# Performance work log

Hardware: AMD Instinct MI355X
Metric: run time of the kernel (lower is better)

The kernel has to match this reference:

```python
import jax, jax.numpy as jnp
import numpy as np

NUM_CLASSES = 80
NUM_ANCHORS = 3  # len(anchor_mask)
STRIDE = 8.0
# anchors[mask=0,1,2] = (12,16),(19,36),(40,28), divided by stride
ANCHOR_W = jnp.array([12.0, 19.0, 40.0], dtype=jnp.float32) / STRIDE
ANCHOR_H = jnp.array([16.0, 36.0, 28.0], dtype=jnp.float32) / STRIDE


def setup_inputs() -> dict:
    key = jax.random.key(0)
    output = jax.random.normal(key, (16, NUM_ANCHORS * (5 + NUM_CLASSES), 76, 76), dtype=jnp.float32)
    return {"output": output}


def reference(output):
    B, C_total, H, W = output.shape
    A, C = NUM_ANCHORS, NUM_CLASSES
    o = output.reshape(B, A, 5 + C, H, W)

    bxy = jax.nn.sigmoid(o[:, :, 0:2])          # [B,A,2,H,W]
    bwh = jnp.exp(o[:, :, 2:4])                 # [B,A,2,H,W]
    det_confs = jax.nn.sigmoid(o[:, :, 4])      # [B,A,H,W]
    cls_confs = jax.nn.softmax(o[:, :, 5:], axis=2)  # softmax over class dim, [B,A,C,H,W]

    grid_x = jnp.arange(W, dtype=jnp.float32)[None, None, None, :]
    grid_y = jnp.arange(H, dtype=jnp.float32)[None, None, :, None]
    aw = ANCHOR_W[None, :, None, None]
    ah = ANCHOR_H[None, :, None, None]

    bx = (bxy[:, :, 0] + grid_x) / W            # [B,A,H,W]
    by = (bxy[:, :, 1] + grid_y) / H
    bw = (bwh[:, :, 0] * aw) / W
    bh = (bwh[:, :, 1] * ah) / H

    boxes = jnp.stack([bx, by, bw, bh], axis=-1).reshape(B, A * H * W, 4)
    cls_flat = cls_confs.transpose(0, 1, 3, 4, 2).reshape(B, A * H * W, C)
    confs = cls_flat * det_confs.reshape(B, A * H * W, 1)
    return boxes, confs
```

## Files before the change

### kernel.cpp

```cpp
#include <hip/hip_runtime.h>

#define HW_   5776
#define W_    76
#define NC_   80
#define NA_   3
#define NB_   16
#define NCH_  85

__device__ __forceinline__ float sigmoidf_(float x) {
    return 1.0f / (1.0f + __expf(-x));
}

__global__ __launch_bounds__(256) void yolo_kernel(const float* __restrict__ in,
                                                   float* __restrict__ out) {
    const int p = blockIdx.x * 256 + threadIdx.x;
    if (p >= HW_) return;
    const int a = blockIdx.y;
    const int b = blockIdx.z;

    const float aw3[3] = {1.5f, 2.375f, 5.0f};
    const float ah3[3] = {2.0f, 4.5f, 3.5f};
    const float invW = 1.0f / 76.0f;

    const float* src = in + (size_t)(b * NA_ + a) * NCH_ * HW_ + p;
    float v[NCH_];
#pragma unroll
    for (int ch = 0; ch < NCH_; ++ch) {
        v[ch] = src[(size_t)ch * HW_];
    }

    const int x = p % W_;
    const int y = p / W_;

    const float bx  = (sigmoidf_(v[0]) + (float)x) * invW;
    const float by  = (sigmoidf_(v[1]) + (float)y) * invW;
    const float bw  = __expf(v[2]) * (aw3[a] * invW);
    const float bh  = __expf(v[3]) * (ah3[a] * invW);
    const float det = sigmoidf_(v[4]);

    float m = v[5];
#pragma unroll
    for (int c = 1; c < NC_; ++c) m = fmaxf(m, v[5 + c]);
    float s = 0.0f;
#pragma unroll
    for (int c = 0; c < NC_; ++c) {
        v[5 + c] = __expf(v[5 + c] - m);
        s += v[5 + c];
    }
    const float scale = det / s;

    const size_t idx = (size_t)a * HW_ + (size_t)p;
    float4* boxout = (float4*)out + (size_t)b * (NA_ * HW_) + idx;
    *boxout = make_float4(bx, by, bw, bh);

    float* conf = out + (size_t)NB_ * NA_ * HW_ * 4
                      + ((size_t)b * (NA_ * HW_) + idx) * NC_;
#pragma unroll
    for (int c = 0; c < NC_; c += 4) {
        float4 val = make_float4(v[5 + c]     * scale,
                                 v[5 + c + 1] * scale,
                                 v[5 + c + 2] * scale,
                                 v[5 + c + 3] * scale);
        *(float4*)(conf + c) = val;
    }
}

extern "C" void kernel_launch(void* const* d_in, const int* in_sizes, int n_in,
                              void* d_out, int out_size, void* d_ws, size_t ws_size,
                              hipStream_t stream) {
    const float* in = (const float*)d_in[0];
    float* out = (float*)d_out;
    dim3 grid((HW_ + 255) / 256, NA_, NB_);
    yolo_kernel<<<grid, 256, 0, stream>>>(in, out);
}
```

Baseline: 192.7 us.

## Split class softmax across two half-wavefronts per position with flat grid

Each position is now handled by two lanes, each taking 40 of the 80 class channels. Max and sum are combined with a cross-half shuffle. The grid is flattened over batch, anchor and position, which removes the partial tail blocks of the old per-slab grid. The goal is lower register pressure and more memory-level parallelism for a bandwidth-bound kernel. In exchange, both halves redundantly load and compute the box terms, and each half wavefront reads only 32 contiguous floats per load.

Result: faster. 184.7 us (-4.1%).

```diff
diff --git a/kernel.cpp b/kernel.cpp
--- a/kernel.cpp
+++ b/kernel.cpp
@@ -6,6 +6,7 @@
 #define NA_   3
 #define NB_   16
 #define NCH_  85
+#define NPOS  (NB_ * NA_ * HW_)
 
 __device__ __forceinline__ float sigmoidf_(float x) {
     return 1.0f / (1.0f + __expf(-x));
@@ -13,55 +14,61 @@
 
 __global__ __launch_bounds__(256) void yolo_kernel(const float* __restrict__ in,
                                                    float* __restrict__ out) {
-    const int p = blockIdx.x * 256 + threadIdx.x;
-    if (p >= HW_) return;
-    const int a = blockIdx.y;
-    const int b = blockIdx.z;
+    const int tid  = threadIdx.x;
+    const int lane = tid & 63;
+    const int wv   = tid >> 6;
+    const int half = lane >> 5;
+    const int P = blockIdx.x * 128 + wv * 32 + (lane & 31);
+
+    const int slab = P / HW_;
+    const int p    = P - slab * HW_;
+    const int a    = slab % NA_;
 
     const float aw3[3] = {1.5f, 2.375f, 5.0f};
     const float ah3[3] = {2.0f, 4.5f, 3.5f};
     const float invW = 1.0f / 76.0f;
 
-    const float* src = in + (size_t)(b * NA_ + a) * NCH_ * HW_ + p;
-    float v[NCH_];
+    const float* src = in + (size_t)slab * (NCH_ * HW_) + p;
+
+    const float b0 = src[0 * (size_t)HW_];
+    const float b1 = src[1 * (size_t)HW_];
+    const float b2 = src[2 * (size_t)HW_];
+    const float b3 = src[3 * (size_t)HW_];
+    const float b4 = src[4 * (size_t)HW_];
+
+    const float* csrc = src + (size_t)(5 + half * 40) * HW_;
+    float v[40];
 #pragma unroll
-    for (int ch = 0; ch < NCH_; ++ch) {
-        v[ch] = src[(size_t)ch * HW_];
-    }
+    for (int c = 0; c < 40; ++c) v[c] = csrc[(size_t)c * HW_];
 
     const int x = p % W_;
     const int y = p / W_;
+    const float bx  = (sigmoidf_(b0) + (float)x) * invW;
+    const float by  = (sigmoidf_(b1) + (float)y) * invW;
+    const float bw  = __expf(b2) * (aw3[a] * invW);
+    const float bh  = __expf(b3) * (ah3[a] * invW);
+    const float det = sigmoidf_(b4);
 
-    const float bx  = (sigmoidf_(v[0]) + (float)x) * invW;
-    const float by  = (sigmoidf_(v[1]) + (float)y) * invW;
-    const float bw  = __expf(v[2]) * (aw3[a] * invW);
-    const float bh  = __expf(v[3]) * (ah3[a] * invW);
-    const float det = sigmoidf_(v[4]);
-
-    float m = v[5];
+    float m = v[0];
 #pragma unroll
-    for (int c = 1; c < NC_; ++c) m = fmaxf(m, v[5 + c]);
+    for (int c = 1; c < 40; ++c) m = fmaxf(m, v[c]);
+    m = fmaxf(m, __shfl_xor(m, 32));
     float s = 0.0f;
 #pragma unroll
-    for (int c = 0; c < NC_; ++c) {
-        v[5 + c] = __expf(v[5 + c] - m);
-        s += v[5 + c];
-    }
+    for (int c = 0; c < 40; ++c) { v[c] = __expf(v[c] - m); s += v[c]; }
+    s += __shfl_xor(s, 32);
     const float scale = det / s;
 
-    const size_t idx = (size_t)a * HW_ + (size_t)p;
-    float4* boxout = (float4*)out + (size_t)b * (NA_ * HW_) + idx;
-    *boxout = make_float4(bx, by, bw, bh);
-
-    float* conf = out + (size_t)NB_ * NA_ * HW_ * 4
-                      + ((size_t)b * (NA_ * HW_) + idx) * NC_;
+    if (half == 0) {
+        ((float4*)out)[P] = make_float4(bx, by, bw, bh);
+    }
+    float* conf = out + (size_t)NPOS * 4 + (size_t)P * NC_ + half * 40;
 #pragma unroll
-    for (int c = 0; c < NC_; c += 4) {
-        float4 val = make_float4(v[5 + c]     * scale,
-                                 v[5 + c + 1] * scale,
-                                 v[5 + c + 2] * scale,
-                                 v[5 + c + 3] * scale);
-        *(float4*)(conf + c) = val;
+    for (int c = 0; c < 40; c += 4) {
+        *(float4*)(conf + c) = make_float4(v[c]     * scale,
+                                           v[c + 1] * scale,
+                                           v[c + 2] * scale,
+                                           v[c + 3] * scale);
     }
 }
 
@@ -70,6 +77,6 @@
                               hipStream_t stream) {
     const float* in = (const float*)d_in[0];
     float* out = (float*)d_out;
-    dim3 grid((HW_ + 255) / 256, NA_, NB_);
-    yolo_kernel<<<grid, 256, 0, stream>>>(in, out);
+    const int nblocks = NPOS / 128;
+    yolo_kernel<<<nblocks, 256, 0, stream>>>(in, out);
 }
```
